# Optimization experiments

Hardware: AMD Instinct MI355X
Metric: run time of the kernel (lower is better)

The kernel has to match this reference:

```python
import jax, jax.numpy as jnp
import numpy as np

EPS = 1e-5

def layer_norm(x, scale, bias):
    mu = jnp.mean(x, axis=-1, keepdims=True)
    var = jnp.var(x, axis=-1, keepdims=True)
    return (x - mu) * jax.lax.rsqrt(var + EPS) * scale + bias

def setup_inputs() -> dict:
    key = jax.random.key(0)
    ks = jax.random.split(key, 12)
    b, l, c_in, c_mid = 1, 512, 128, 128
    act = jax.random.normal(ks[0], (b, l, l, c_in), dtype=jnp.float32)
    mask = jnp.ones((b, l), dtype=jnp.float32)
    sd_in = 1.0 / np.sqrt(c_in)
    sd_mid = 1.0 / np.sqrt(c_mid)
    return {
        "act": act,
        "mask": mask,
        "norm_scale": jnp.ones((c_in,), jnp.float32),
        "norm_bias": jnp.zeros((c_in,), jnp.float32),
        "w_left": jax.random.normal(ks[1], (c_in, c_mid), jnp.float32) * sd_in,
        "b_left": jnp.zeros((c_mid,), jnp.float32),
        "w_right": jax.random.normal(ks[2], (c_in, c_mid), jnp.float32) * sd_in,
        "b_right": jnp.zeros((c_mid,), jnp.float32),
        "w_lgate": jax.random.normal(ks[3], (c_in, c_mid), jnp.float32) * sd_in,
        "b_lgate": jnp.ones((c_mid,), jnp.float32),  # gate init bias=1
        "w_rgate": jax.random.normal(ks[4], (c_in, c_mid), jnp.float32) * sd_in,
        "b_rgate": jnp.ones((c_mid,), jnp.float32),
        "fnorm_scale": jnp.ones((c_mid,), jnp.float32),
        "fnorm_bias": jnp.zeros((c_mid,), jnp.float32),
        "w_out": jax.random.normal(ks[5], (c_mid, c_in), jnp.float32) * sd_mid,
        "b_out": jnp.zeros((c_in,), jnp.float32),
        "w_fgate": jax.random.normal(ks[6], (c_in, c_in), jnp.float32) * sd_in,
        "b_fgate": jnp.ones((c_in,), jnp.float32),
    }

def reference(act, mask, norm_scale, norm_bias, w_left, b_left, w_right, b_right,
              w_lgate, b_lgate, w_rgate, b_rgate, fnorm_scale, fnorm_bias,
              w_out, b_out, w_fgate, b_fgate):
    # pair_mask: (b,l,l,1)
    pair_mask = mask[:, :, None, None] * mask[:, None, :, None]
    x = layer_norm(act, norm_scale, norm_bias)  # (b,l,l,c_in)
    input_act = x
    left = (x @ w_left + b_left) * pair_mask
    right = (x @ w_right + b_right) * pair_mask
    left = left * jax.nn.sigmoid(x @ w_lgate + b_lgate)
    right = right * jax.nn.sigmoid(x @ w_rgate + b_rgate)
    # per_row orientation
    out = jnp.einsum('bikc,bjkc->bijc', left, right)
    out = layer_norm(out, fnorm_scale, fnorm_bias)
    out = out @ w_out + b_out
    out = out * jax.nn.sigmoid(input_act @ w_fgate + b_fgate)
    return out
```

## Files before the change

### kernel.cpp

```cpp
#include <hip/hip_runtime.h>
#include <hip/hip_bf16.h>
#include <stdint.h>

#define LDIM 512
#define CDIM 128
#define NPOS (LDIM*LDIM)

typedef __attribute__((ext_vector_type(8))) short bf16x8;
typedef __attribute__((ext_vector_type(4))) float f32x4;

__device__ __forceinline__ unsigned short f2bf(float f) {
  union { __hip_bfloat16 h; unsigned short u; } cv;
  cv.h = __float2bfloat16(f);
  return cv.u;
}

__device__ __forceinline__ float bf2f(unsigned short u) {
  union { unsigned int i; float f; } cv; cv.i = ((unsigned int)u) << 16; return cv.f;
}

__device__ __forceinline__ float sigm(float x) { return 1.0f / (1.0f + __expf(-x)); }

__device__ __forceinline__ void gl_lds16(const unsigned short* g, unsigned short* l) {
  __builtin_amdgcn_global_load_lds(
      (const __attribute__((address_space(1))) unsigned int*)g,
      (__attribute__((address_space(3))) unsigned int*)l, 16, 0, 0);
}

__global__ __launch_bounds__(256) void k_prep(
    const float* w0, const float* w1, const float* w2,
    const float* w3, const float* w4, const float* w5,
    unsigned short* wtall) {
  __shared__ float tmp[CDIM*CDIM];
  const float* w = (blockIdx.x==0)?w0:(blockIdx.x==1)?w1:(blockIdx.x==2)?w2:
                   (blockIdx.x==3)?w3:(blockIdx.x==4)?w4:w5;
  int t = threadIdx.x;
  #pragma unroll
  for (int m = 0; m < 16; ++m)
    ((float4*)tmp)[m*256 + t] = ((const float4*)w)[m*256 + t];
  __syncthreads();
  unsigned short* out = wtall + (size_t)blockIdx.x * (CDIM*CDIM);
  #pragma unroll
  for (int m = 0; m < 8; ++m) {
    int oc = m*256 + t;
    int n = oc >> 4, sc = oc & 15;
    int s = sc ^ (n & 7);
    union { unsigned short u[8]; uint4 v; } pk;
    #pragma unroll
    for (int e = 0; e < 8; ++e) pk.u[e] = f2bf(tmp[(s*8 + e)*CDIM + n]);
    *(uint4*)(out + (size_t)oc*8) = pk.v;
  }
}

__global__ __launch_bounds__(256,8) void k_ln(
    const float* __restrict__ act,
    const float* __restrict__ nscale, const float* __restrict__ nbias,
    unsigned short* __restrict__ xbf) {
  const int t = threadIdx.x;
  const int pos = blockIdx.x * 64 + (t >> 2), qq = t & 3;
  const int s = pos & 7;

  float4 av[8];
  const float4* ap = (const float4*)(act + (size_t)pos*CDIM);
  #pragma unroll
  for (int cc = 0; cc < 4; ++cc) {
    int ch = cc*4 + qq;
    av[cc*2]     = ap[ch*2];
    av[cc*2 + 1] = ap[ch*2 + 1];
  }

  float sm = 0.f, s2 = 0.f;
  #pragma unroll
  for (int j = 0; j < 8; ++j) {
    float4 v = av[j];
    sm += v.x + v.y + v.z + v.w;
    s2 += v.x*v.x + v.y*v.y + v.z*v.z + v.w*v.w;
  }
  sm += __shfl_xor(sm, 1); s2 += __shfl_xor(s2, 1);
  sm += __shfl_xor(sm, 2); s2 += __shfl_xor(s2, 2);
  float mu = sm * 0.0078125f;
  float rs = rsqrtf(fmaxf(s2 * 0.0078125f - mu*mu, 0.f) + 1e-5f);

  unsigned short* xp = xbf + (size_t)pos * CDIM;
  #pragma unroll
  for (int cc = 0; cc < 4; ++cc) {
    int ch = cc*4 + qq;
    union { unsigned short u[8]; uint4 v; } pk;
    #pragma unroll
    for (int e2 = 0; e2 < 2; ++e2) {
      float4 v = av[cc*2 + e2];
      float4 fs = ((const float4*)nscale)[ch*2 + e2];
      float4 fb = ((const float4*)nbias)[ch*2 + e2];
      int b = e2*4;
      pk.u[b+0] = f2bf((v.x - mu)*rs*fs.x + fb.x);
      pk.u[b+1] = f2bf((v.y - mu)*rs*fs.y + fb.y);
      pk.u[b+2] = f2bf((v.z - mu)*rs*fs.z + fb.z);
      pk.u[b+3] = f2bf((v.w - mu)*rs*fs.w + fb.w);
    }
    int slot = ch ^ s;
    *(uint4*)(xp + slot*8) = pk.v;
  }
}

__global__ __launch_bounds__(512,4) void k_proj(
    const unsigned short* __restrict__ xbf,
    const float* __restrict__ mask,
    const float* __restrict__ b_left, const float* __restrict__ b_lgate,
    const float* __restrict__ b_right, const float* __restrict__ b_rgate,
    const unsigned short* __restrict__ wtall,
    unsigned short* __restrict__ leftT,
    unsigned short* __restrict__ rightT) {
  __shared__ unsigned short WB[128*128];
  __shared__ unsigned short xs[2][64*128];
  const int t = threadIdx.x, wave = t >> 6, lane = t & 63;
  const int fr = lane & 15, kg = lane >> 4;
  const int rg = wave >> 2;
  const int cg = wave & 3;

  const int side = blockIdx.x >> 9;
  const unsigned short* W = wtall + (size_t)side * 2 * 16384;
  const float* bvp = side ? b_right : b_left;
  const float* bgp = side ? b_rgate : b_lgate;
  unsigned short* dst = side ? rightT : leftT;

  const int tile0 = (blockIdx.x & 511) * 8;

  #pragma unroll
  for (int m = 0; m < 4; ++m) {
    int qb = m*512 + wave*64;
    gl_lds16(W + (size_t)(qb + lane)*8, WB + qb*8);
  }
  #pragma unroll
  for (int m = 0; m < 2; ++m) {
    int qb = m*512 + wave*64;
    gl_lds16(xbf + (size_t)tile0*64*CDIM + (size_t)(qb + lane)*8, xs[0] + qb*8);
  }
  __syncthreads();

  bf16x8 bv[2][4];
  #pragma unroll
  for (int nf = 0; nf < 2; ++nf) {
    int n = cg*32 + nf*16 + fr;
    #pragma unroll
    for (int ks = 0; ks < 4; ++ks)
      bv[nf][ks] = *(const bf16x8*)(WB + n*128 + (((ks*4 + kg) ^ (n & 7)) * 8));
  }
  __syncthreads();

  #pragma unroll
  for (int m = 0; m < 4; ++m) {
    int qb = m*512 + wave*64;
    gl_lds16(W + 16384 + (size_t)(qb + lane)*8, WB + qb*8);
  }
  __syncthreads();

  const f32x4 fz = {0.f,0.f,0.f,0.f};
  int cur = 0;
  for (int tt = 0; tt < 8; ++tt) {
    const int p0 = (tile0 + tt) * 64;
    if (tt < 7) {
      #pragma unroll
      for (int m = 0; m < 2; ++m) {
        int qb = m*512 + wave*64;
        gl_lds16(xbf + (size_t)(p0 + 64)*CDIM + (size_t)(qb + lane)*8, xs[cur^1] + qb*8);
      }
    }

    bf16x8 afr[2][4];
    #pragma unroll
    for (int rf = 0; rf < 2; ++rf) {
      int ar = rg*32 + rf*16 + fr;
      #pragma unroll
      for (int ks = 0; ks < 4; ++ks)
        afr[rf][ks] = *(const bf16x8*)(xs[cur] + ar*128 + (((ks*4 + kg) ^ (ar & 7)) * 8));
    }

    f32x4 accV[2][2], accG[2][2];
    #pragma unroll
    for (int rf = 0; rf < 2; ++rf)
      #pragma unroll
      for (int nf = 0; nf < 2; ++nf) { accV[rf][nf] = fz; accG[rf][nf] = fz; }

    #pragma unroll
    for (int nf = 0; nf < 2; ++nf) {
      int n = cg*32 + nf*16 + fr;
      const unsigned short* Wp = WB + n*128;
      #pragma unroll
      for (int ks = 0; ks < 4; ++ks) {
        bf16x8 bgf = *(const bf16x8*)(Wp + (((ks*4 + kg) ^ (n & 7)) * 8));
        accG[0][nf] = __builtin_amdgcn_mfma_f32_16x16x32_bf16(afr[0][ks], bgf, accG[0][nf], 0,0,0);
        accG[1][nf] = __builtin_amdgcn_mfma_f32_16x16x32_bf16(afr[1][ks], bgf, accG[1][nf], 0,0,0);
      }
    }
    #pragma unroll
    for (int nf = 0; nf < 2; ++nf)
      #pragma unroll
      for (int ks = 0; ks < 4; ++ks) {
        accV[0][nf] = __builtin_amdgcn_mfma_f32_16x16x32_bf16(afr[0][ks], bv[nf][ks], accV[0][nf], 0,0,0);
        accV[1][nf] = __builtin_amdgcn_mfma_f32_16x16x32_bf16(afr[1][ks], bv[nf][ks], accV[1][nf], 0,0,0);
      }

    float mi = mask[p0 >> 9];
    union { unsigned short u[4]; uint2 v; } pl[2][2];
    #pragma unroll
    for (int rf = 0; rf < 2; ++rf) {
      const int rbase = rg*32 + rf*16 + kg*4;
      float pm[4];
      #pragma unroll
      for (int jj = 0; jj < 4; ++jj)
        pm[jj] = mi * mask[(p0 & 511) + rbase + jj];
      #pragma unroll
      for (int nf = 0; nf < 2; ++nf) {
        int n = cg*32 + nf*16 + fr;
        float bvn = bvp[n], bgn = bgp[n];
        #pragma unroll
        for (int jj = 0; jj < 4; ++jj)
          pl[rf][nf].u[jj] = f2bf((accV[rf][nf][jj] + bvn) * pm[jj] * sigm(accG[rf][nf][jj] + bgn));
      }
    }

    if (tt < 7) __syncthreads();

    #pragma unroll
    for (int rf = 0; rf < 2; ++rf) {
      const int rbase = rg*32 + rf*16 + kg*4;
      #pragma unroll
      for (int nf = 0; nf < 2; ++nf) {
        int n = cg*32 + nf*16 + fr;
        *(uint2*)(dst + (size_t)n*NPOS + p0 + rbase) = pl[rf][nf].v;
      }
    }
    cur ^= 1;
  }
}

__global__ __launch_bounds__(256,2) void k_einsum(
    const unsigned short* __restrict__ leftT,
    const unsigned short* __restrict__ rightT,
    unsigned short* __restrict__ eout) {
  __shared__ unsigned short At[2][128*64];
  __shared__ unsigned short Bt[2][128*64];
  const int t = threadIdx.x, wave = t >> 6, lane = t & 63;
  int fl = (blockIdx.x & 7) * 256 + (blockIdx.x >> 3);
  const int c = fl >> 4;
  const int i0 = ((fl >> 2) & 3) * 128, j0 = (fl & 3) * 128;
  const unsigned short* Lp = leftT + (size_t)c * NPOS;
  const unsigned short* Rp = rightT + (size_t)c * NPOS;
  const int wrow = (wave >> 1) * 64, wcol = (wave & 1) * 64;
  const int kg = lane >> 4, fr = lane & 15;

  f32x4 acc[4][4];
  const f32x4 fz = {0.f,0.f,0.f,0.f};
  #pragma unroll
  for (int a = 0; a < 4; ++a)
    #pragma unroll
    for (int b = 0; b < 4; ++b) acc[a][b] = fz;

  #define STAGE(buf, kt) do {                                              \
    _Pragma("unroll")                                                      \
    for (int m = 0; m < 4; ++m) {                                          \
      int qb = m*256 + wave*64;                                            \
      int qq = qb + lane;                                                  \
      int r = qq >> 3;                                                     \
      int kk = (qq & 7) ^ (r & 7);                                         \
      gl_lds16(Lp + ((size_t)(i0 + r) << 9) + (kt)*64 + kk*8, At[buf] + qb*8); \
      gl_lds16(Rp + ((size_t)(j0 + r) << 9) + (kt)*64 + kk*8, Bt[buf] + qb*8); \
    }                                                                      \
  } while (0)

  STAGE(0, 0);
  __syncthreads();
  int cur = 0;
  for (int kt = 0; kt < 8; ++kt) {
    if (kt < 7) STAGE(cur ^ 1, kt + 1);
    #pragma unroll
    for (int ks = 0; ks < 2; ++ks) {
      bf16x8 af[4], bfr[4];
      #pragma unroll
      for (int mf = 0; mf < 4; ++mf) {
        int r = wrow + mf*16 + fr;
        af[mf] = *(const bf16x8*)(At[cur] + r*64 + (((ks*4 + kg) ^ (r & 7)) * 8));
      }
      #pragma unroll
      for (int nf = 0; nf < 4; ++nf) {
        int r = wcol + nf*16 + fr;
        bfr[nf] = *(const bf16x8*)(Bt[cur] + r*64 + (((ks*4 + kg) ^ (r & 7)) * 8));
      }
      #pragma unroll
      for (int mf = 0; mf < 4; ++mf)
        #pragma unroll
        for (int nf = 0; nf < 4; ++nf)
          acc[mf][nf] = __builtin_amdgcn_mfma_f32_16x16x32_bf16(af[mf], bfr[nf], acc[mf][nf], 0,0,0);
    }
    __syncthreads();
    cur ^= 1;
  }
  #undef STAGE

  unsigned short* bounce = &At[0][0];
  const int rb = kg << 2;
  #pragma unroll
  for (int mf = 0; mf < 4; ++mf) {
    #pragma unroll
    for (int nf = 0; nf < 4; ++nf) {
      #pragma unroll
      for (int jj = 0; jj < 4; ++jj) {
        int ri = wrow + mf*16 + rb + jj;
        int ci = wcol + nf*16 + fr;
        bounce[ri*128 + (((ci >> 3) ^ (ri & 7)) << 3) + (ci & 7)] = f2bf(acc[mf][nf][jj]);
      }
    }
  }
  __syncthreads();
  unsigned short* op = eout + (size_t)c * NPOS;
  #pragma unroll
  for (int rr = 0; rr < 8; ++rr) {
    int flat = rr*256 + t;
    int row = flat >> 4, ch = flat & 15;
    uint4 v = *(const uint4*)(bounce + row*128 + ((ch ^ (row & 7)) << 3));
    *(uint4*)(op + (size_t)(i0 + row)*LDIM + j0 + ch*8) = v;
  }
}

__global__ __launch_bounds__(512,2) void k_stageC(
    const unsigned short* __restrict__ eout,
    const unsigned short* __restrict__ xbf,
    const unsigned short* __restrict__ wtall,
    const float* __restrict__ fns, const float* __restrict__ fnb,
    const float* __restrict__ b_out, const float* __restrict__ b_fg,
    float* __restrict__ outp) {
  __shared__ unsigned short WB[2][128*128];
  __shared__ unsigned short xs[2][64*128];
  __shared__ unsigned short es[2][64*128];
  __shared__ float psum[2][8][64];
  const int t = threadIdx.x, wave = t >> 6, lane = t & 63;
  const int fr = lane & 15, kg = lane >> 4;
  const int rg = wave >> 1, cg = wave & 1;
  const int ar = rg*16 + fr;
  const int rbase = rg*16 + kg*4;

  #pragma unroll
  for (int m = 0; m < 4; ++m) {
    int qb = m*512 + wave*64;
    gl_lds16(wtall + 5*16384 + (size_t)(qb + lane)*8, WB[0] + qb*8);
    gl_lds16(wtall + 4*16384 + (size_t)(qb + lane)*8, WB[1] + qb*8);
  }

  const int tile0 = blockIdx.x * 8;
  uint4 xr0, xr1, er0, er1;
  {
    const uint4* xsrc = (const uint4*)(xbf + (size_t)tile0*64*CDIM);
    xr0 = xsrc[t]; xr1 = xsrc[512 + t];
    const unsigned short* eb = eout + (size_t)tile0*64;
    er0 = *(const uint4*)(eb + (size_t)(t >> 3)*NPOS + (t & 7)*8);
    er1 = *(const uint4*)(eb + (size_t)(64 + (t >> 3))*NPOS + (t & 7)*8);
  }
  *(uint4*)(xs[0] + t*8) = xr0; *(uint4*)(xs[0] + 4096 + t*8) = xr1;
  *(uint4*)(es[0] + t*8) = er0; *(uint4*)(es[0] + 4096 + t*8) = er1;

  int cur = 0;
  const f32x4 fz = {0.f,0.f,0.f,0.f};
  for (int tt = 0; tt < 8; ++tt) {
    const int p0 = (tile0 + tt) * 64;
    __syncthreads();

    if (tt < 7) {
      const uint4* xsrc = (const uint4*)(xbf + (size_t)(p0 + 64)*CDIM);
      xr0 = xsrc[t]; xr1 = xsrc[512 + t];
      const unsigned short* eb = eout + (size_t)(p0 + 64);
      er0 = *(const uint4*)(eb + (size_t)(t >> 3)*NPOS + (t & 7)*8);
      er1 = *(const uint4*)(eb + (size_t)(64 + (t >> 3))*NPOS + (t & 7)*8);
    }

    float ev[16];
    #pragma unroll
    for (int j = 0; j < 16; ++j)
      ev[j] = bf2f(es[cur][(wave*16 + j)*64 + lane]);
    float s = 0.f, s2 = 0.f;
    #pragma unroll
    for (int j = 0; j < 16; ++j) { s += ev[j]; s2 += ev[j]*ev[j]; }
    psum[0][wave][lane] = s; psum[1][wave][lane] = s2;
    __syncthreads();
    float st = 0.f, s2t = 0.f;
    #pragma unroll
    for (int w = 0; w < 8; ++w) { st += psum[0][w][lane]; s2t += psum[1][w][lane]; }
    float mu = st * 0.0078125f;
    float rs = rsqrtf(fmaxf(s2t * 0.0078125f - mu*mu, 0.f) + 1e-5f);

    bf16x8 afr[4];
    #pragma unroll
    for (int ks = 0; ks < 4; ++ks)
      afr[ks] = *(const bf16x8*)(xs[cur] + ar*128 + (((ks*4 + kg) ^ (ar & 7)) * 8));

    f32x4 accG[4], accY[4];
    #pragma unroll
    for (int nf = 0; nf < 4; ++nf) {
      accG[nf] = fz;
      int n = cg*64 + nf*16 + fr;
      #pragma unroll
      for (int ks = 0; ks < 4; ++ks) {
        bf16x8 b = *(const bf16x8*)(WB[0] + n*128 + (((ks*4 + kg) ^ (n & 7)) * 8));
        accG[nf] = __builtin_amdgcn_mfma_f32_16x16x32_bf16(afr[ks], b, accG[nf], 0,0,0);
      }
    }

    #pragma unroll
    for (int k = 0; k < 2; ++k) {
      union { unsigned short u[8]; uint4 v; } pk;
      #pragma unroll
      for (int e4 = 0; e4 < 2; ++e4) {
        float4 fsv = ((const float4*)fns)[wave*4 + k*2 + e4];
        float4 fbv = ((const float4*)fnb)[wave*4 + k*2 + e4];
        int j = k*8 + e4*4;
        pk.u[e4*4+0] = f2bf((ev[j+0]-mu)*rs*fsv.x + fbv.x);
        pk.u[e4*4+1] = f2bf((ev[j+1]-mu)*rs*fsv.y + fbv.y);
        pk.u[e4*4+2] = f2bf((ev[j+2]-mu)*rs*fsv.z + fbv.z);
        pk.u[e4*4+3] = f2bf((ev[j+3]-mu)*rs*fsv.w + fbv.w);
      }
      int ch = wave*2 + k;
      int slot = ch ^ (lane & 7);
      *(uint4*)(es[cur] + lane*128 + slot*8) = pk.v;
    }
    __syncthreads();

    bf16x8 yfr[4];
    #pragma unroll
    for (int ks = 0; ks < 4; ++ks)
      yfr[ks] = *(const bf16x8*)(es[cur] + ar*128 + (((ks*4 + kg) ^ (ar & 7)) * 8));
    #pragma unroll
    for (int nf = 0; nf < 4; ++nf) {
      accY[nf] = fz;
      int n = cg*64 + nf*16 + fr;
      #pragma unroll
      for (int ks = 0; ks < 4; ++ks) {
        bf16x8 b = *(const bf16x8*)(WB[1] + n*128 + (((ks*4 + kg) ^ (n & 7)) * 8));
        accY[nf] = __builtin_amdgcn_mfma_f32_16x16x32_bf16(yfr[ks], b, accY[nf], 0,0,0);
      }
    }

    #pragma unroll
    for (int nf = 0; nf < 4; ++nf) {
      int n = cg*64 + nf*16 + fr;
      float bo = b_out[n], bfg = b_fg[n];
      #pragma unroll
      for (int jj = 0; jj < 4; ++jj) {
        float val = (accY[nf][jj] + bo) * sigm(accG[nf][jj] + bfg);
        outp[(size_t)(p0 + rbase + jj)*CDIM + n] = val;
      }
    }

    if (tt < 7) {
      *(uint4*)(xs[cur^1] + t*8) = xr0; *(uint4*)(xs[cur^1] + 4096 + t*8) = xr1;
      *(uint4*)(es[cur^1] + t*8) = er0; *(uint4*)(es[cur^1] + 4096 + t*8) = er1;
      cur ^= 1;
    }
  }
}

extern "C" void kernel_launch(void* const* d_in, const int* in_sizes, int n_in,
                              void* d_out, int out_size, void* d_ws, size_t ws_size,
                              hipStream_t stream) {
  const float* act  = (const float*)d_in[0];
  const float* mask = (const float*)d_in[1];
  const float* nsc  = (const float*)d_in[2];
  const float* nbi  = (const float*)d_in[3];
  const float* w_l  = (const float*)d_in[4];
  const float* b_l  = (const float*)d_in[5];
  const float* w_r  = (const float*)d_in[6];
  const float* b_r  = (const float*)d_in[7];
  const float* w_lg = (const float*)d_in[8];
  const float* b_lg = (const float*)d_in[9];
  const float* w_rg = (const float*)d_in[10];
  const float* b_rg = (const float*)d_in[11];
  const float* fns  = (const float*)d_in[12];
  const float* fnb  = (const float*)d_in[13];
  const float* w_o  = (const float*)d_in[14];
  const float* b_o  = (const float*)d_in[15];
  const float* w_fg = (const float*)d_in[16];
  const float* b_fg = (const float*)d_in[17];
  float* outp = (float*)d_out;

  char* ws = (char*)d_ws;
  unsigned short* xbf    = (unsigned short*)ws;
  unsigned short* leftT  = (unsigned short*)(ws + ((size_t)64 << 20));
  unsigned short* rightT = (unsigned short*)(ws + ((size_t)128 << 20));
  unsigned short* eout   = (unsigned short*)(ws + ((size_t)192 << 20));
  unsigned short* wtall  = (unsigned short*)(ws + ((size_t)320 << 20));

  k_prep<<<6, 256, 0, stream>>>(w_l, w_lg, w_r, w_rg, w_o, w_fg, wtall);
  k_ln<<<NPOS/64, 256, 0, stream>>>(act, nsc, nbi, xbf);
  k_proj<<<1024, 512, 0, stream>>>(xbf, mask, b_l, b_lg, b_r, b_rg, wtall, leftT, rightT);
  k_einsum<<<2048, 256, 0, stream>>>(leftT, rightT, eout);
  k_stageC<<<512, 512, 0, stream>>>(eout, xbf, wtall, fns, fnb, b_o, b_fg, outp);
}
```

Measured before the change: 248.3 us.

## Fuse input layernorm into projection kernel, computing LN per tile in registers

Removes the standalone layernorm kernel. The projection kernel now loads fp32 activations itself, normalizes them in registers with an 8-lane shuffle reduction, and writes the bf16 result into its shared-memory tile. The left-side blocks also write the normalized tile to global memory for the final stage. This drops one launch and one round trip of the bf16 activations. In exchange, both sides read the fp32 input (so activation reads double) and the LN work is repeated per side, adding register pressure and latency to the projection loop.

Result: slower. 368.8 us (+48.5%).

```diff
diff --git a/kernel.cpp b/kernel.cpp
--- a/kernel.cpp
+++ b/kernel.cpp
@@ -52,65 +52,17 @@
   }
 }
 
-__global__ __launch_bounds__(256,8) void k_ln(
+__global__ __launch_bounds__(512,4) void k_proj(
     const float* __restrict__ act,
     const float* __restrict__ nscale, const float* __restrict__ nbias,
-    unsigned short* __restrict__ xbf) {
-  const int t = threadIdx.x;
-  const int pos = blockIdx.x * 64 + (t >> 2), qq = t & 3;
-  const int s = pos & 7;
-
-  float4 av[8];
-  const float4* ap = (const float4*)(act + (size_t)pos*CDIM);
-  #pragma unroll
-  for (int cc = 0; cc < 4; ++cc) {
-    int ch = cc*4 + qq;
-    av[cc*2]     = ap[ch*2];
-    av[cc*2 + 1] = ap[ch*2 + 1];
-  }
-
-  float sm = 0.f, s2 = 0.f;
-  #pragma unroll
-  for (int j = 0; j < 8; ++j) {
-    float4 v = av[j];
-    sm += v.x + v.y + v.z + v.w;
-    s2 += v.x*v.x + v.y*v.y + v.z*v.z + v.w*v.w;
-  }
-  sm += __shfl_xor(sm, 1); s2 += __shfl_xor(s2, 1);
-  sm += __shfl_xor(sm, 2); s2 += __shfl_xor(s2, 2);
-  float mu = sm * 0.0078125f;
-  float rs = rsqrtf(fmaxf(s2 * 0.0078125f - mu*mu, 0.f) + 1e-5f);
-
-  unsigned short* xp = xbf + (size_t)pos * CDIM;
-  #pragma unroll
-  for (int cc = 0; cc < 4; ++cc) {
-    int ch = cc*4 + qq;
-    union { unsigned short u[8]; uint4 v; } pk;
-    #pragma unroll
-    for (int e2 = 0; e2 < 2; ++e2) {
-      float4 v = av[cc*2 + e2];
-      float4 fs = ((const float4*)nscale)[ch*2 + e2];
-      float4 fb = ((const float4*)nbias)[ch*2 + e2];
-      int b = e2*4;
-      pk.u[b+0] = f2bf((v.x - mu)*rs*fs.x + fb.x);
-      pk.u[b+1] = f2bf((v.y - mu)*rs*fs.y + fb.y);
-      pk.u[b+2] = f2bf((v.z - mu)*rs*fs.z + fb.z);
-      pk.u[b+3] = f2bf((v.w - mu)*rs*fs.w + fb.w);
-    }
-    int slot = ch ^ s;
-    *(uint4*)(xp + slot*8) = pk.v;
-  }
-}
-
-__global__ __launch_bounds__(512,4) void k_proj(
-    const unsigned short* __restrict__ xbf,
     const float* __restrict__ mask,
     const float* __restrict__ b_left, const float* __restrict__ b_lgate,
     const float* __restrict__ b_right, const float* __restrict__ b_rgate,
     const unsigned short* __restrict__ wtall,
+    unsigned short* __restrict__ xbf,
     unsigned short* __restrict__ leftT,
     unsigned short* __restrict__ rightT) {
-  __shared__ unsigned short WB[128*128];
+  __shared__ unsigned short WBg[128*128];
   __shared__ unsigned short xs[2][64*128];
   const int t = threadIdx.x, wave = t >> 6, lane = t & 63;
   const int fr = lane & 15, kg = lane >> 4;
@@ -125,16 +77,56 @@
 
   const int tile0 = (blockIdx.x & 511) * 8;
 
+  const int posl = t >> 3, q8 = t & 7;
+  const float4 ns0a = ((const float4*)nscale)[q8*2];
+  const float4 ns0b = ((const float4*)nscale)[q8*2 + 1];
+  const float4 ns1a = ((const float4*)nscale)[16 + q8*2];
+  const float4 ns1b = ((const float4*)nscale)[17 + q8*2];
+  const float4 nb0a = ((const float4*)nbias)[q8*2];
+  const float4 nb0b = ((const float4*)nbias)[q8*2 + 1];
+  const float4 nb1a = ((const float4*)nbias)[16 + q8*2];
+  const float4 nb1b = ((const float4*)nbias)[17 + q8*2];
+
+  float4 av0, av1, av2, av3;
+  #define LOAD_ACT(P0) do {                                                 \
+    const float4* ap_ = (const float4*)(act + (size_t)((P0) + posl)*CDIM);  \
+    av0 = ap_[q8*2]; av1 = ap_[q8*2 + 1];                                   \
+    av2 = ap_[16 + q8*2]; av3 = ap_[17 + q8*2];                             \
+  } while (0)
+
+  uint4 pk0, pk1;
+  #define LN_FINISH() do {                                                  \
+    float s_ = 0.f, s2_ = 0.f;                                              \
+    { float4 v_;                                                            \
+      v_ = av0; s_ += v_.x+v_.y+v_.z+v_.w; s2_ += v_.x*v_.x+v_.y*v_.y+v_.z*v_.z+v_.w*v_.w; \
+      v_ = av1; s_ += v_.x+v_.y+v_.z+v_.w; s2_ += v_.x*v_.x+v_.y*v_.y+v_.z*v_.z+v_.w*v_.w; \
+      v_ = av2; s_ += v_.x+v_.y+v_.z+v_.w; s2_ += v_.x*v_.x+v_.y*v_.y+v_.z*v_.z+v_.w*v_.w; \
+      v_ = av3; s_ += v_.x+v_.y+v_.z+v_.w; s2_ += v_.x*v_.x+v_.y*v_.y+v_.z*v_.z+v_.w*v_.w; } \
+    s_ += __shfl_xor(s_, 1); s2_ += __shfl_xor(s2_, 1);                     \
+    s_ += __shfl_xor(s_, 2); s2_ += __shfl_xor(s2_, 2);                     \
+    s_ += __shfl_xor(s_, 4); s2_ += __shfl_xor(s2_, 4);                     \
+    float mu_ = s_ * 0.0078125f;                                            \
+    float rs_ = rsqrtf(fmaxf(s2_ * 0.0078125f - mu_*mu_, 0.f) + 1e-5f);     \
+    union { unsigned short u[8]; uint4 v; } w0_, w1_;                       \
+    w0_.u[0]=f2bf((av0.x-mu_)*rs_*ns0a.x+nb0a.x); w0_.u[1]=f2bf((av0.y-mu_)*rs_*ns0a.y+nb0a.y); \
+    w0_.u[2]=f2bf((av0.z-mu_)*rs_*ns0a.z+nb0a.z); w0_.u[3]=f2bf((av0.w-mu_)*rs_*ns0a.w+nb0a.w); \
+    w0_.u[4]=f2bf((av1.x-mu_)*rs_*ns0b.x+nb0b.x); w0_.u[5]=f2bf((av1.y-mu_)*rs_*ns0b.y+nb0b.y); \
+    w0_.u[6]=f2bf((av1.z-mu_)*rs_*ns0b.z+nb0b.z); w0_.u[7]=f2bf((av1.w-mu_)*rs_*ns0b.w+nb0b.w); \
+    w1_.u[0]=f2bf((av2.x-mu_)*rs_*ns1a.x+nb1a.x); w1_.u[1]=f2bf((av2.y-mu_)*rs_*ns1a.y+nb1a.y); \
+    w1_.u[2]=f2bf((av2.z-mu_)*rs_*ns1a.z+nb1a.z); w1_.u[3]=f2bf((av2.w-mu_)*rs_*ns1a.w+nb1a.w); \
+    w1_.u[4]=f2bf((av3.x-mu_)*rs_*ns1b.x+nb1b.x); w1_.u[5]=f2bf((av3.y-mu_)*rs_*ns1b.y+nb1b.y); \
+    w1_.u[6]=f2bf((av3.z-mu_)*rs_*ns1b.z+nb1b.z); w1_.u[7]=f2bf((av3.w-mu_)*rs_*ns1b.w+nb1b.w); \
+    pk0 = w0_.v; pk1 = w1_.v;                                               \
+  } while (0)
+
+  const int slot0 = q8 ^ (posl & 7);
+
   #pragma unroll
   for (int m = 0; m < 4; ++m) {
     int qb = m*512 + wave*64;
-    gl_lds16(W + (size_t)(qb + lane)*8, WB + qb*8);
-  }
-  #pragma unroll
-  for (int m = 0; m < 2; ++m) {
-    int qb = m*512 + wave*64;
-    gl_lds16(xbf + (size_t)tile0*64*CDIM + (size_t)(qb + lane)*8, xs[0] + qb*8);
-  }
+    gl_lds16(W + (size_t)(qb + lane)*8, WBg + qb*8);
+  }
+  LOAD_ACT(tile0*64);
   __syncthreads();
 
   bf16x8 bv[2][4];
@@ -143,14 +135,22 @@
     int n = cg*32 + nf*16 + fr;
     #pragma unroll
     for (int ks = 0; ks < 4; ++ks)
-      bv[nf][ks] = *(const bf16x8*)(WB + n*128 + (((ks*4 + kg) ^ (n & 7)) * 8));
+      bv[nf][ks] = *(const bf16x8*)(WBg + n*128 + (((ks*4 + kg) ^ (n & 7)) * 8));
   }
   __syncthreads();
 
   #pragma unroll
   for (int m = 0; m < 4; ++m) {
     int qb = m*512 + wave*64;
-    gl_lds16(W + 16384 + (size_t)(qb + lane)*8, WB + qb*8);
+    gl_lds16(W + 16384 + (size_t)(qb + lane)*8, WBg + qb*8);
+  }
+  LN_FINISH();
+  *(uint4*)(xs[0] + posl*128 + slot0*8)      = pk0;
+  *(uint4*)(xs[0] + posl*128 + slot0*8 + 64) = pk1;
+  if (side == 0) {
+    unsigned short* xp = xbf + (size_t)(tile0*64 + posl)*CDIM;
+    *(uint4*)(xp + slot0*8)      = pk0;
+    *(uint4*)(xp + slot0*8 + 64) = pk1;
   }
   __syncthreads();
 
@@ -158,13 +158,7 @@
   int cur = 0;
   for (int tt = 0; tt < 8; ++tt) {
     const int p0 = (tile0 + tt) * 64;
-    if (tt < 7) {
-      #pragma unroll
-      for (int m = 0; m < 2; ++m) {
-        int qb = m*512 + wave*64;
-        gl_lds16(xbf + (size_t)(p0 + 64)*CDIM + (size_t)(qb + lane)*8, xs[cur^1] + qb*8);
-      }
-    }
+    if (tt < 7) LOAD_ACT(p0 + 64);
 
     bf16x8 afr[2][4];
     #pragma unroll
@@ -184,7 +178,7 @@
     #pragma unroll
     for (int nf = 0; nf < 2; ++nf) {
       int n = cg*32 + nf*16 + fr;
-      const unsigned short* Wp = WB + n*128;
+      const unsigned short* Wp = WBg + n*128;
       #pragma unroll
       for (int ks = 0; ks < 4; ++ks) {
         bf16x8 bgf = *(const bf16x8*)(Wp + (((ks*4 + kg) ^ (n & 7)) * 8));
@@ -219,6 +213,12 @@
       }
     }
 
+    if (tt < 7) {
+      LN_FINISH();
+      *(uint4*)(xs[cur^1] + posl*128 + slot0*8)      = pk0;
+      *(uint4*)(xs[cur^1] + posl*128 + slot0*8 + 64) = pk1;
+    }
+
     if (tt < 7) __syncthreads();
 
     #pragma unroll
@@ -230,8 +230,15 @@
         *(uint2*)(dst + (size_t)n*NPOS + p0 + rbase) = pl[rf][nf].v;
       }
     }
+    if (side == 0 && tt < 7) {
+      unsigned short* xp = xbf + (size_t)(p0 + 64 + posl)*CDIM;
+      *(uint4*)(xp + slot0*8)      = pk0;
+      *(uint4*)(xp + slot0*8 + 64) = pk1;
+    }
     cur ^= 1;
   }
+  #undef LOAD_ACT
+  #undef LN_FINISH
 }
 
 __global__ __launch_bounds__(256,2) void k_einsum(
@@ -488,8 +495,8 @@
   unsigned short* wtall  = (unsigned short*)(ws + ((size_t)320 << 20));
 
   k_prep<<<6, 256, 0, stream>>>(w_l, w_lg, w_r, w_rg, w_o, w_fg, wtall);
-  k_ln<<<NPOS/64, 256, 0, stream>>>(act, nsc, nbi, xbf);
-  k_proj<<<1024, 512, 0, stream>>>(xbf, mask, b_l, b_lg, b_r, b_rg, wtall, leftT, rightT);
+  k_proj<<<1024, 512, 0, stream>>>(act, nsc, nbi, mask, b_l, b_lg, b_r, b_rg,
+                                   wtall, xbf, leftT, rightT);
   k_einsum<<<2048, 256, 0, stream>>>(leftT, rightT, eout);
   k_stageC<<<512, 512, 0, stream>>>(eout, xbf, wtall, fns, fnb, b_o, b_fg, outp);
 }
```
